# Performance work log

Measured on AMD Instinct MI355X. Metric: run time of the kernel, lower is better.

Reference implementation:

```python
import jax, jax.numpy as jnp
import numpy as np

H = 32          # query heads
KV = 8          # key/value heads
HD = 128        # head_dim
EPS = 1e-6
SCALE = HD ** -0.5


def _rms_norm(x, w):
    # per-head RMSNorm over last dim in fp32
    xf = x.astype(jnp.float32)
    var = jnp.mean(xf * xf, axis=-1, keepdims=True)
    return (w * (xf * jax.lax.rsqrt(var + EPS))).astype(x.dtype)


def _rotate_half(x):
    x1, x2 = jnp.split(x, 2, axis=-1)
    return jnp.concatenate([-x2, x1], axis=-1)


def setup_inputs() -> dict:
    key = jax.random.key(0)
    ks = jax.random.split(key, 8)
    B, S, D = 1, 2048, 4096
    hidden_states = jax.random.normal(ks[0], (B, S, D), dtype=jnp.float32)
    # rotary tables (half head dim), realistic frequencies
    pos = jnp.arange(S, dtype=jnp.float32)
    inv_freq = 1.0 / (1e6 ** (jnp.arange(0, HD, 2, dtype=jnp.float32) / HD))
    ang = pos[:, None] * inv_freq[None, :]          # [S, HD/2]
    cos = jnp.broadcast_to(jnp.cos(ang)[None], (B, S, HD // 2))
    sin = jnp.broadcast_to(jnp.sin(ang)[None], (B, S, HD // 2))
    # additive causal mask [B,1,S,S]
    causal = jnp.tril(jnp.ones((S, S), dtype=bool))
    attention_mask = jnp.where(causal, 0.0, -1e9).astype(jnp.float32)[None, None]
    attention_mask = jnp.broadcast_to(attention_mask, (B, 1, S, S))
    std = 0.02
    Wq = jax.random.normal(ks[1], (H * HD, D), dtype=jnp.float32) * std
    Wk = jax.random.normal(ks[2], (KV * HD, D), dtype=jnp.float32) * std
    Wv = jax.random.normal(ks[3], (KV * HD, D), dtype=jnp.float32) * std
    Wo = jax.random.normal(ks[4], (D, H * HD), dtype=jnp.float32) * std
    q_norm_w = jnp.ones((HD,), dtype=jnp.float32)
    k_norm_w = jnp.ones((HD,), dtype=jnp.float32)
    return {"hidden_states": hidden_states, "cos": cos, "sin": sin,
            "attention_mask": attention_mask, "Wq": Wq, "Wk": Wk, "Wv": Wv,
            "Wo": Wo, "q_norm_w": q_norm_w, "k_norm_w": k_norm_w}


def reference(hidden_states, cos, sin, attention_mask, Wq, Wk, Wv, Wo, q_norm_w, k_norm_w):
    B, S, D = hidden_states.shape
    # QKV projections (no bias), reshape to heads, per-head RMSNorm on q/k
    q = (hidden_states @ Wq.T).reshape(B, S, H, HD)
    k = (hidden_states @ Wk.T).reshape(B, S, KV, HD)
    v = (hidden_states @ Wv.T).reshape(B, S, KV, HD)
    q = _rms_norm(q, q_norm_w).transpose(0, 2, 1, 3)   # [B,H,S,HD]
    k = _rms_norm(k, k_norm_w).transpose(0, 2, 1, 3)   # [B,KV,S,HD]
    v = v.transpose(0, 2, 1, 3)                        # [B,KV,S,HD]
    # RoPE: cos/sin [B,S,HD/2] -> [B,1,S,HD]
    cos2 = jnp.concatenate([cos, cos], axis=-1)[:, None]
    sin2 = jnp.concatenate([sin, sin], axis=-1)[:, None]
    q = q * cos2 + _rotate_half(q) * sin2
    k = k * cos2 + _rotate_half(k) * sin2
    # GQA repeat kv
    n_rep = H // KV
    k = jnp.repeat(k, n_rep, axis=1)                   # [B,H,S,HD]
    v = jnp.repeat(v, n_rep, axis=1)
    # eager attention, fp32 softmax
    scores = jnp.einsum('bhqd,bhkd->bhqk', q, k) * SCALE + attention_mask
    probs = jax.nn.softmax(scores.astype(jnp.float32), axis=-1).astype(q.dtype)
    attn = jnp.einsum('bhqk,bhkd->bhqd', probs, v)
    attn = attn.transpose(0, 2, 1, 3).reshape(B, S, H * HD)
    return attn @ Wo.T
```

## Files before the change

### kernel.cpp

```cpp
#include <hip/hip_runtime.h>
#include <hip/hip_bf16.h>


#define S_LEN 2048
#define D_MODEL 4096
#define NH 32
#define NKV 8
#define HD 128
#define EPS 1e-6f
#define SCALE 0.08838834764831845f
#define NEG_BIG (-1e30f)

typedef __bf16 bf16_t;
typedef __bf16 bf16x8 __attribute__((ext_vector_type(8)));
typedef __bf16 bf16x4 __attribute__((ext_vector_type(4)));
typedef float f32x4 __attribute__((ext_vector_type(4)));

__device__ __forceinline__ bool input_is_bf16(const void* qw) {
    return ((*(const unsigned*)qw) & 0xFFFFu) == 0x3F80u;
}

__device__ __forceinline__ void gload_lds16(const void* g, void* l) {
    __builtin_amdgcn_global_load_lds(
        (const __attribute__((address_space(1))) void*)g,
        (__attribute__((address_space(3))) void*)l, 16, 0, 0);
}

template<bool BF16>
__device__ __forceinline__ float ld1(const void* p, size_t i) {
    if constexpr (BF16) return (float)((const bf16_t*)p)[i];
    else return ((const float*)p)[i];
}
template<bool BF16>
__device__ __forceinline__ void st1(void* p, size_t i, float v) {
    if constexpr (BF16) ((bf16_t*)p)[i] = (bf16_t)v;
    else ((float*)p)[i] = v;
}

__device__ __forceinline__ bf16x8 cvt8(const float* src) {
    float4 a = *(const float4*)src, b = *(const float4*)(src + 4);
    bf16x8 r;
    r[0] = (bf16_t)a.x; r[1] = (bf16_t)a.y; r[2] = (bf16_t)a.z; r[3] = (bf16_t)a.w;
    r[4] = (bf16_t)b.x; r[5] = (bf16_t)b.y; r[6] = (bf16_t)b.z; r[7] = (bf16_t)b.w;
    return r;
}

__global__ __launch_bounds__(256) void conv_kernel(const void* src, const void* qw,
                                                   bf16_t* __restrict__ dst) {
    size_t i = ((size_t)blockIdx.x * 256 + threadIdx.x) * 8;
    if (input_is_bf16(qw)) {
        *(bf16x8*)&dst[i] = *(const bf16x8*)((const bf16_t*)src + i);
    } else {
        *(bf16x8*)&dst[i] = cvt8((const float*)src + i);
    }
}

template<bool BF16>
__device__ __forceinline__ void stage_b(const void* W, size_t nrow0, int k0,
                                        bf16_t* lds_b, int tid, int lane, int w) {
    if constexpr (BF16) {
        const bf16_t* Wb = (const bf16_t*)W + nrow0 * D_MODEL;
        #pragma unroll
        for (int i = 0; i < 2; ++i) {
            int r16 = w * 2 + i;
            gload_lds16(Wb + (size_t)(r16 * 16 + (lane >> 2)) * D_MODEL + k0 + (lane & 3) * 8,
                        &lds_b[r16 * 512]);
        }
    } else {
        const float* Wf = (const float*)W + nrow0 * D_MODEL;
        #pragma unroll
        for (int j = 0; j < 2; ++j) {
            int e = j * 2048 + tid * 8;
            int row = e >> 5, kk = e & 31;
            *(bf16x8*)&lds_b[e] = cvt8(Wf + (size_t)row * D_MODEL + k0 + kk);
        }
    }
}

template<bool BF16>
__device__ void qkv_body(
    const bf16_t* __restrict__ hsb, const void* cosp, const void* sinp,
    const void* Wq, const void* Wk, const void* Wv,
    const void* qw, const void* kw,
    bf16_t* __restrict__ qn, bf16_t* __restrict__ kn, bf16_t* __restrict__ vt,
    bf16_t* lds_a, bf16_t* lds_b)
{
    const int tid = threadIdx.x;
    const int lane = tid & 63;
    const int w = tid >> 6;
    const int c = lane & 15;
    const int g = lane >> 4;
    const int m0 = blockIdx.x * 128;
    const int slot = blockIdx.y;

    const void* Wbase; int type, h;
    if (slot < 32)      { type = 0; h = slot;      Wbase = Wq; }
    else if (slot < 40) { type = 1; h = slot - 32; Wbase = Wk; }
    else                { type = 2; h = slot - 40; Wbase = Wv; }
    const size_t nrow0 = (size_t)h * HD;

    f32x4 acc[2][8] = {};

    for (int k0 = 0; k0 < D_MODEL; k0 += 32) {
        __syncthreads();
        #pragma unroll
        for (int i = 0; i < 2; ++i) {
            int r16 = w * 2 + i;
            gload_lds16(hsb + (size_t)(m0 + r16 * 16 + (lane >> 2)) * D_MODEL + k0 + (lane & 3) * 8,
                        &lds_a[r16 * 512]);
        }
        stage_b<BF16>(Wbase, nrow0, k0, lds_b, tid, lane, w);
        __syncthreads();

        bf16x8 af0 = *(const bf16x8*)&lds_a[(w * 32 + c) * 32 + g * 8];
        bf16x8 af1 = *(const bf16x8*)&lds_a[(w * 32 + 16 + c) * 32 + g * 8];
        #pragma unroll
        for (int ni = 0; ni < 8; ++ni) {
            bf16x8 bfr = *(const bf16x8*)&lds_b[(ni * 16 + c) * 32 + g * 8];
            acc[0][ni] = __builtin_amdgcn_mfma_f32_16x16x32_bf16(af0, bfr, acc[0][ni], 0, 0, 0);
            acc[1][ni] = __builtin_amdgcn_mfma_f32_16x16x32_bf16(af1, bfr, acc[1][ni], 0, 0, 0);
        }
    }

    if (type == 2) {
        #pragma unroll
        for (int mi = 0; mi < 2; ++mi) {
            int s = m0 + w * 32 + mi * 16 + g * 4;
            #pragma unroll
            for (int ni = 0; ni < 8; ++ni) {
                bf16x4 pk;
                #pragma unroll
                for (int r = 0; r < 4; ++r) pk[r] = (bf16_t)acc[mi][ni][r];
                *(bf16x4*)&vt[((size_t)h * HD + ni * 16 + c) * S_LEN + s] = pk;
            }
        }
        return;
    }

    const void* nw = (type == 0) ? qw : kw;
    bf16_t* outb = (type == 0) ? (qn + (size_t)h * S_LEN * HD)
                               : (kn + (size_t)h * S_LEN * HD);
    #pragma unroll
    for (int mi = 0; mi < 2; ++mi) {
        float ss[4];
        #pragma unroll
        for (int r = 0; r < 4; ++r) {
            float p = 0.f;
            #pragma unroll
            for (int ni = 0; ni < 8; ++ni) p += acc[mi][ni][r] * acc[mi][ni][r];
            p += __shfl_xor(p, 1); p += __shfl_xor(p, 2);
            p += __shfl_xor(p, 4); p += __shfl_xor(p, 8);
            ss[r] = rsqrtf(p * (1.f / HD) + EPS);
        }
        float v[8][4];
        #pragma unroll
        for (int ni = 0; ni < 8; ++ni) {
            float wg = ld1<BF16>(nw, ni * 16 + c);
            #pragma unroll
            for (int r = 0; r < 4; ++r) v[ni][r] = acc[mi][ni][r] * ss[r] * wg;
        }
        #pragma unroll
        for (int r = 0; r < 4; ++r) {
            int s = m0 + w * 32 + mi * 16 + g * 4 + r;
            #pragma unroll
            for (int t = 0; t < 4; ++t) {
                int nn = t * 16 + c;
                float co = ld1<BF16>(cosp, (size_t)s * 64 + nn);
                float si = ld1<BF16>(sinp, (size_t)s * 64 + nn);
                float x1 = v[t][r], x2 = v[t + 4][r];
                v[t][r]     = x1 * co - x2 * si;
                v[t + 4][r] = x2 * co + x1 * si;
            }
        }
        #pragma unroll
        for (int t = 0; t < 8; ++t)
            #pragma unroll
            for (int r = 0; r < 4; ++r) {
                int s = m0 + w * 32 + mi * 16 + g * 4 + r;
                outb[(size_t)s * HD + t * 16 + c] = (bf16_t)v[t][r];
            }
    }
}

__global__ __launch_bounds__(256) void qkv_kernel(
    const bf16_t* __restrict__ hsb, const void* cosp, const void* sinp,
    const void* Wq, const void* Wk, const void* Wv,
    const void* qw, const void* kw,
    bf16_t* __restrict__ qn, bf16_t* __restrict__ kn, bf16_t* __restrict__ vt)
{
    __shared__ bf16_t lds_a[128 * 32];
    __shared__ bf16_t lds_b[128 * 32];
    if (input_is_bf16(qw))
        qkv_body<true>(hsb, cosp, sinp, Wq, Wk, Wv, qw, kw, qn, kn, vt, lds_a, lds_b);
    else
        qkv_body<false>(hsb, cosp, sinp, Wq, Wk, Wv, qw, kw, qn, kn, vt, lds_a, lds_b);
}

__global__ __launch_bounds__(256) void attn_kernel(
    const bf16_t* __restrict__ qn, const bf16_t* __restrict__ kn,
    const bf16_t* __restrict__ vt, bf16_t* __restrict__ attnb)
{
    __shared__ bf16_t lds_k[32 * 128];
    __shared__ bf16_t lds_v[128 * 32];

    const int lane = threadIdx.x & 63;
    const int w = threadIdx.x >> 6;
    const int c = lane & 15;
    const int g = lane >> 4;
    const int h = blockIdx.y;
    const int hk = h >> 2;
    const int xa = blockIdx.x;
    const int lr = lane >> 2;
    const int lk = (lane & 3) * 8;

    const int qrow0 = xa * 64 + w * 16;
    const int qrow1 = (31 - xa) * 64 + w * 16;
    const int kmaxA = xa * 64 + 64;
    const int kmaxB = (31 - xa) * 64 + 64;

    const bf16_t* kb_base = kn + (size_t)hk * S_LEN * HD;
    const bf16_t* vt_base = vt + (size_t)hk * HD * S_LEN;

    bf16x8 qf[2][4];
    #pragma unroll
    for (int ks = 0; ks < 4; ++ks) {
        qf[0][ks] = *(const bf16x8*)(qn + ((size_t)h * S_LEN + qrow0 + c) * HD + ks * 32 + g * 8);
        qf[1][ks] = *(const bf16x8*)(qn + ((size_t)h * S_LEN + qrow1 + c) * HD + ks * 32 + g * 8);
    }

    f32x4 o[2][8] = {};
    float m_cur[2] = {NEG_BIG, NEG_BIG};
    float l_cur[2] = {0.f, 0.f};

    for (int kb = 0; kb < kmaxB; kb += 32) {
        const bool liveA = (kb < kmaxA);
        __syncthreads();
        #pragma unroll
        for (int i = 0; i < 2; ++i) {
            int t16 = w * 2 + i;
            gload_lds16(kb_base + (size_t)(kb + t16 * 4 + g) * HD + c * 8,
                        &lds_k[t16 * 512]);
            gload_lds16(vt_base + (size_t)(t16 * 16 + lr) * S_LEN + kb + lk,
                        &lds_v[t16 * 512]);
        }
        __syncthreads();

        float p[2][2][4];
        #pragma unroll
        for (int u = 0; u < 2; ++u) {
            f32x4 sacc0 = {}, sacc1 = {};
            #pragma unroll
            for (int ks = 0; ks < 4; ++ks) {
                bf16x8 kf = *(const bf16x8*)&lds_k[(u * 16 + c) * 128 + ks * 32 + g * 8];
                if (liveA)
                    sacc0 = __builtin_amdgcn_mfma_f32_16x16x32_bf16(kf, qf[0][ks], sacc0, 0, 0, 0);
                sacc1 = __builtin_amdgcn_mfma_f32_16x16x32_bf16(kf, qf[1][ks], sacc1, 0, 0, 0);
            }
            #pragma unroll
            for (int r = 0; r < 4; ++r) {
                int key_abs = kb + u * 16 + g * 4 + r;
                p[0][u][r] = (key_abs <= qrow0 + c) ? sacc0[r] * SCALE : NEG_BIG;
                p[1][u][r] = (key_abs <= qrow1 + c) ? sacc1[r] * SCALE : NEG_BIG;
            }
        }

        bf16x8 pb[2];
        #pragma unroll
        for (int qt = 0; qt < 2; ++qt) {
            if (qt == 0 && !liveA) continue;
            float mx = NEG_BIG;
            #pragma unroll
            for (int u = 0; u < 2; ++u)
                #pragma unroll
                for (int r = 0; r < 4; ++r) mx = fmaxf(mx, p[qt][u][r]);
            mx = fmaxf(mx, __shfl_xor(mx, 16));
            mx = fmaxf(mx, __shfl_xor(mx, 32));
            float m_new = fmaxf(m_cur[qt], mx);
            float alpha = __expf(m_cur[qt] - m_new);
            float lsum = 0.f;
            #pragma unroll
            for (int u = 0; u < 2; ++u)
                #pragma unroll
                for (int r = 0; r < 4; ++r) {
                    float e = __expf(p[qt][u][r] - m_new);
                    p[qt][u][r] = e;
                    lsum += e;
                }
            lsum += __shfl_xor(lsum, 16);
            lsum += __shfl_xor(lsum, 32);
            l_cur[qt] = l_cur[qt] * alpha + lsum;
            m_cur[qt] = m_new;
            #pragma unroll
            for (int dt = 0; dt < 8; ++dt) o[qt][dt] *= alpha;
            #pragma unroll
            for (int j = 0; j < 8; ++j) {
                int src = (((g * 2 + (j >> 2)) & 3) << 4) | c;
                float v0 = __shfl(p[qt][0][j & 3], src);
                float v1 = __shfl(p[qt][1][j & 3], src);
                pb[qt][j] = (bf16_t)((g >= 2) ? v1 : v0);
            }
        }
        #pragma unroll
        for (int dt = 0; dt < 8; ++dt) {
            bf16x8 vf = *(const bf16x8*)&lds_v[(dt * 16 + c) * 32 + g * 8];
            if (liveA)
                o[0][dt] = __builtin_amdgcn_mfma_f32_16x16x32_bf16(vf, pb[0], o[0][dt], 0, 0, 0);
            o[1][dt] = __builtin_amdgcn_mfma_f32_16x16x32_bf16(vf, pb[1], o[1][dt], 0, 0, 0);
        }
    }

    #pragma unroll
    for (int qt = 0; qt < 2; ++qt) {
        float inv_l = 1.f / l_cur[qt];
        int q = (qt == 0 ? qrow0 : qrow1) + c;
        #pragma unroll
        for (int dt = 0; dt < 8; ++dt) {
            bf16x4 pk;
            #pragma unroll
            for (int r = 0; r < 4; ++r) pk[r] = (bf16_t)(o[qt][dt][r] * inv_l);
            *(bf16x4*)&attnb[(size_t)q * D_MODEL + h * HD + dt * 16 + g * 4] = pk;
        }
    }
}

template<bool BF16>
__device__ void out_body(const bf16_t* __restrict__ attnb, const void* Wo,
                         void* outp, bf16_t* lds_a, bf16_t* lds_b)
{
    const int tid = threadIdx.x;
    const int lane = tid & 63;
    const int w = tid >> 6;
    const int c = lane & 15;
    const int g = lane >> 4;
    const int wm = w >> 1, wn = w & 1;
    const int m0 = blockIdx.x * 128, n0 = blockIdx.y * 128;

    f32x4 acc[4][4] = {};
    for (int k0 = 0; k0 < D_MODEL; k0 += 32) {
        __syncthreads();
        #pragma unroll
        for (int i = 0; i < 2; ++i) {
            int r16 = w * 2 + i;
            gload_lds16(attnb + (size_t)(m0 + r16 * 16 + (lane >> 2)) * D_MODEL + k0 + (lane & 3) * 8,
                        &lds_a[r16 * 512]);
        }
        stage_b<BF16>(Wo, (size_t)n0, k0, lds_b, tid, lane, w);
        __syncthreads();

        bf16x8 af[4], bfr[4];
        #pragma unroll
        for (int i = 0; i < 4; ++i) {
            af[i]  = *(const bf16x8*)&lds_a[(wm * 64 + i * 16 + c) * 32 + g * 8];
            bfr[i] = *(const bf16x8*)&lds_b[(wn * 64 + i * 16 + c) * 32 + g * 8];
        }
        #pragma unroll
        for (int mi = 0; mi < 4; ++mi)
            #pragma unroll
            for (int ni = 0; ni < 4; ++ni)
                acc[mi][ni] = __builtin_amdgcn_mfma_f32_16x16x32_bf16(af[mi], bfr[ni], acc[mi][ni], 0, 0, 0);
    }
    #pragma unroll
    for (int mi = 0; mi < 4; ++mi)
        #pragma unroll
        for (int ni = 0; ni < 4; ++ni)
            #pragma unroll
            for (int r = 0; r < 4; ++r)
                st1<BF16>(outp, (size_t)(m0 + wm * 64 + mi * 16 + g * 4 + r) * D_MODEL
                                 + n0 + wn * 64 + ni * 16 + c, acc[mi][ni][r]);
}

__global__ __launch_bounds__(256) void out_kernel(
    const bf16_t* __restrict__ attnb, const void* Wo, const void* qw, void* outp)
{
    __shared__ bf16_t lds_a[128 * 32];
    __shared__ bf16_t lds_b[128 * 32];
    if (input_is_bf16(qw)) out_body<true>(attnb, Wo, outp, lds_a, lds_b);
    else                   out_body<false>(attnb, Wo, outp, lds_a, lds_b);
}

extern "C" void kernel_launch(void* const* d_in, const int* in_sizes, int n_in,
                              void* d_out, int out_size, void* d_ws, size_t ws_size,
                              hipStream_t stream) {
    const void* hs   = d_in[0];
    const void* cosp = d_in[1];
    const void* sinp = d_in[2];
    const void* Wq = d_in[4];
    const void* Wk = d_in[5];
    const void* Wv = d_in[6];
    const void* Wo = d_in[7];
    const void* qw = d_in[8];
    const void* kw = d_in[9];

    const size_t NEED = 16777216ull + 16777216ull + 4194304ull + 4194304ull;
    if (ws_size < NEED) return;

    char* ws = (char*)d_ws;
    bf16_t* buf0 = (bf16_t*)(ws);
    bf16_t* qn   = (bf16_t*)(ws + 16777216);
    bf16_t* kn   = (bf16_t*)(ws + 2 * 16777216);
    bf16_t* vt   = (bf16_t*)(ws + 2 * 16777216 + 4194304);

    conv_kernel<<<dim3(4096), 256, 0, stream>>>(hs, qw, buf0);
    qkv_kernel<<<dim3(16, 48), 256, 0, stream>>>(buf0, cosp, sinp, Wq, Wk, Wv, qw, kw,
                                                 qn, kn, vt);
    attn_kernel<<<dim3(16, 32), 256, 0, stream>>>(qn, kn, vt, buf0);
    out_kernel<<<dim3(16, 32), 256, 0, stream>>>(buf0, Wo, qw, d_out);
}
```

Baseline: 762.4 us.

## Pre-convert weights to bf16 and double-buffer LDS in GEMM kernels

Adds a kernel that converts Wq, Wk, Wv and Wo to bf16 in workspace once per call. The QKV and output GEMMs can then stage weights with direct global-to-LDS loads instead of converting fp32 inline in every block. Both GEMM loops also get double-buffered LDS so the next K-tile loads while the current one computes, dropping one barrier per iteration. The cost is an extra full read and write pass over all weights per call, a larger workspace requirement, and double the LDS footprint, which may lower occupancy.

```diff
diff --git a/kernel.cpp b/kernel.cpp
--- a/kernel.cpp
+++ b/kernel.cpp
@@ -55,10 +55,38 @@
     }
 }
 
-template<bool BF16>
-__device__ __forceinline__ void stage_b(const void* W, size_t nrow0, int k0,
+__global__ __launch_bounds__(256) void convw_kernel(
+    const void* Wq, const void* Wk, const void* Wv, const void* Wo,
+    const void* qw, bf16_t* __restrict__ dq, bf16_t* __restrict__ dk,
+    bf16_t* __restrict__ dv, bf16_t* __restrict__ dwo) {
+    int b = blockIdx.x;
+    const void* src; bf16_t* dst; size_t base;
+    if (b < 8192)       { src = Wq; dst = dq;  base = (size_t)b * 2048; }
+    else if (b < 10240) { src = Wk; dst = dk;  base = (size_t)(b - 8192) * 2048; }
+    else if (b < 12288) { src = Wv; dst = dv;  base = (size_t)(b - 10240) * 2048; }
+    else                { src = Wo; dst = dwo; base = (size_t)(b - 12288) * 2048; }
+    size_t i = base + (size_t)threadIdx.x * 8;
+    if (input_is_bf16(qw)) {
+        *(bf16x8*)&dst[i] = *(const bf16x8*)((const bf16_t*)src + i);
+    } else {
+        *(bf16x8*)&dst[i] = cvt8((const float*)src + i);
+    }
+}
+
+__device__ __forceinline__ void stage_a(const bf16_t* __restrict__ src, int m0,
+                                        int k0, bf16_t* lds_a, int lane, int w) {
+    #pragma unroll
+    for (int i = 0; i < 2; ++i) {
+        int r16 = w * 2 + i;
+        gload_lds16(src + (size_t)(m0 + r16 * 16 + (lane >> 2)) * D_MODEL + k0 + (lane & 3) * 8,
+                    &lds_a[r16 * 512]);
+    }
+}
+
+template<bool WB>
+__device__ __forceinline__ void stage_w(const void* W, size_t nrow0, int k0,
                                         bf16_t* lds_b, int tid, int lane, int w) {
-    if constexpr (BF16) {
+    if constexpr (WB) {
         const bf16_t* Wb = (const bf16_t*)W + nrow0 * D_MODEL;
         #pragma unroll
         for (int i = 0; i < 2; ++i) {
@@ -77,7 +105,7 @@
     }
 }
 
-template<bool BF16>
+template<bool BF16, bool WB>
 __device__ void qkv_body(
     const bf16_t* __restrict__ hsb, const void* cosp, const void* sinp,
     const void* Wq, const void* Wk, const void* Wv,
@@ -101,25 +129,29 @@
 
     f32x4 acc[2][8] = {};
 
+    stage_a(hsb, m0, 0, lds_a, lane, w);
+    stage_w<WB>(Wbase, nrow0, 0, lds_b, tid, lane, w);
+    __syncthreads();
+
+    int cur = 0;
     for (int k0 = 0; k0 < D_MODEL; k0 += 32) {
-        __syncthreads();
-        #pragma unroll
-        for (int i = 0; i < 2; ++i) {
-            int r16 = w * 2 + i;
-            gload_lds16(hsb + (size_t)(m0 + r16 * 16 + (lane >> 2)) * D_MODEL + k0 + (lane & 3) * 8,
-                        &lds_a[r16 * 512]);
-        }
-        stage_b<BF16>(Wbase, nrow0, k0, lds_b, tid, lane, w);
-        __syncthreads();
-
-        bf16x8 af0 = *(const bf16x8*)&lds_a[(w * 32 + c) * 32 + g * 8];
-        bf16x8 af1 = *(const bf16x8*)&lds_a[(w * 32 + 16 + c) * 32 + g * 8];
+        int nxt = cur ^ 1;
+        if (k0 + 32 < D_MODEL) {
+            stage_a(hsb, m0, k0 + 32, lds_a + nxt * 4096, lane, w);
+            stage_w<WB>(Wbase, nrow0, k0 + 32, lds_b + nxt * 4096, tid, lane, w);
+        }
+        const bf16_t* la = lds_a + cur * 4096;
+        const bf16_t* lb = lds_b + cur * 4096;
+        bf16x8 af0 = *(const bf16x8*)&la[(w * 32 + c) * 32 + g * 8];
+        bf16x8 af1 = *(const bf16x8*)&la[(w * 32 + 16 + c) * 32 + g * 8];
         #pragma unroll
         for (int ni = 0; ni < 8; ++ni) {
-            bf16x8 bfr = *(const bf16x8*)&lds_b[(ni * 16 + c) * 32 + g * 8];
+            bf16x8 bfr = *(const bf16x8*)&lb[(ni * 16 + c) * 32 + g * 8];
             acc[0][ni] = __builtin_amdgcn_mfma_f32_16x16x32_bf16(af0, bfr, acc[0][ni], 0, 0, 0);
             acc[1][ni] = __builtin_amdgcn_mfma_f32_16x16x32_bf16(af1, bfr, acc[1][ni], 0, 0, 0);
         }
+        __syncthreads();
+        cur = nxt;
     }
 
     if (type == 2) {
@@ -186,14 +218,19 @@
     const bf16_t* __restrict__ hsb, const void* cosp, const void* sinp,
     const void* Wq, const void* Wk, const void* Wv,
     const void* qw, const void* kw,
-    bf16_t* __restrict__ qn, bf16_t* __restrict__ kn, bf16_t* __restrict__ vt)
+    bf16_t* __restrict__ qn, bf16_t* __restrict__ kn, bf16_t* __restrict__ vt,
+    int wconv)
 {
-    __shared__ bf16_t lds_a[128 * 32];
-    __shared__ bf16_t lds_b[128 * 32];
-    if (input_is_bf16(qw))
-        qkv_body<true>(hsb, cosp, sinp, Wq, Wk, Wv, qw, kw, qn, kn, vt, lds_a, lds_b);
-    else
-        qkv_body<false>(hsb, cosp, sinp, Wq, Wk, Wv, qw, kw, qn, kn, vt, lds_a, lds_b);
+    __shared__ bf16_t lds_a[2][128 * 32];
+    __shared__ bf16_t lds_b[2][128 * 32];
+    bool ib = input_is_bf16(qw);
+    if (wconv) {
+        if (ib) qkv_body<true,  true>(hsb, cosp, sinp, Wq, Wk, Wv, qw, kw, qn, kn, vt, &lds_a[0][0], &lds_b[0][0]);
+        else    qkv_body<false, true>(hsb, cosp, sinp, Wq, Wk, Wv, qw, kw, qn, kn, vt, &lds_a[0][0], &lds_b[0][0]);
+    } else {
+        if (ib) qkv_body<true,  true>(hsb, cosp, sinp, Wq, Wk, Wv, qw, kw, qn, kn, vt, &lds_a[0][0], &lds_b[0][0]);
+        else    qkv_body<false, false>(hsb, cosp, sinp, Wq, Wk, Wv, qw, kw, qn, kn, vt, &lds_a[0][0], &lds_b[0][0]);
+    }
 }
 
 __global__ __launch_bounds__(256) void attn_kernel(
@@ -323,7 +360,7 @@
     }
 }
 
-template<bool BF16>
+template<bool BF16, bool WB>
 __device__ void out_body(const bf16_t* __restrict__ attnb, const void* Wo,
                          void* outp, bf16_t* lds_a, bf16_t* lds_b)
 {
@@ -336,28 +373,33 @@
     const int m0 = blockIdx.x * 128, n0 = blockIdx.y * 128;
 
     f32x4 acc[4][4] = {};
+
+    stage_a(attnb, m0, 0, lds_a, lane, w);
+    stage_w<WB>(Wo, (size_t)n0, 0, lds_b, tid, lane, w);
+    __syncthreads();
+
+    int cur = 0;
     for (int k0 = 0; k0 < D_MODEL; k0 += 32) {
-        __syncthreads();
-        #pragma unroll
-        for (int i = 0; i < 2; ++i) {
-            int r16 = w * 2 + i;
-            gload_lds16(attnb + (size_t)(m0 + r16 * 16 + (lane >> 2)) * D_MODEL + k0 + (lane & 3) * 8,
-                        &lds_a[r16 * 512]);
-        }
-        stage_b<BF16>(Wo, (size_t)n0, k0, lds_b, tid, lane, w);
-        __syncthreads();
-
+        int nxt = cur ^ 1;
+        if (k0 + 32 < D_MODEL) {
+            stage_a(attnb, m0, k0 + 32, lds_a + nxt * 4096, lane, w);
+            stage_w<WB>(Wo, (size_t)n0, k0 + 32, lds_b + nxt * 4096, tid, lane, w);
+        }
+        const bf16_t* la = lds_a + cur * 4096;
+        const bf16_t* lb = lds_b + cur * 4096;
         bf16x8 af[4], bfr[4];
         #pragma unroll
         for (int i = 0; i < 4; ++i) {
-            af[i]  = *(const bf16x8*)&lds_a[(wm * 64 + i * 16 + c) * 32 + g * 8];
-            bfr[i] = *(const bf16x8*)&lds_b[(wn * 64 + i * 16 + c) * 32 + g * 8];
+            af[i]  = *(const bf16x8*)&la[(wm * 64 + i * 16 + c) * 32 + g * 8];
+            bfr[i] = *(const bf16x8*)&lb[(wn * 64 + i * 16 + c) * 32 + g * 8];
         }
         #pragma unroll
         for (int mi = 0; mi < 4; ++mi)
             #pragma unroll
             for (int ni = 0; ni < 4; ++ni)
                 acc[mi][ni] = __builtin_amdgcn_mfma_f32_16x16x32_bf16(af[mi], bfr[ni], acc[mi][ni], 0, 0, 0);
+        __syncthreads();
+        cur = nxt;
     }
     #pragma unroll
     for (int mi = 0; mi < 4; ++mi)
@@ -370,12 +412,19 @@
 }
 
 __global__ __launch_bounds__(256) void out_kernel(
-    const bf16_t* __restrict__ attnb, const void* Wo, const void* qw, void* outp)
+    const bf16_t* __restrict__ attnb, const void* Wo, const void* qw, void* outp,
+    int wconv)
 {
-    __shared__ bf16_t lds_a[128 * 32];
-    __shared__ bf16_t lds_b[128 * 32];
-    if (input_is_bf16(qw)) out_body<true>(attnb, Wo, outp, lds_a, lds_b);
-    else                   out_body<false>(attnb, Wo, outp, lds_a, lds_b);
+    __shared__ bf16_t lds_a[2][128 * 32];
+    __shared__ bf16_t lds_b[2][128 * 32];
+    bool ib = input_is_bf16(qw);
+    if (wconv) {
+        if (ib) out_body<true,  true>(attnb, Wo, outp, &lds_a[0][0], &lds_b[0][0]);
+        else    out_body<false, true>(attnb, Wo, outp, &lds_a[0][0], &lds_b[0][0]);
+    } else {
+        if (ib) out_body<true,  true>(attnb, Wo, outp, &lds_a[0][0], &lds_b[0][0]);
+        else    out_body<false, false>(attnb, Wo, outp, &lds_a[0][0], &lds_b[0][0]);
+    }
 }
 
 extern "C" void kernel_launch(void* const* d_in, const int* in_sizes, int n_in,
@@ -391,8 +440,10 @@
     const void* qw = d_in[8];
     const void* kw = d_in[9];
 
-    const size_t NEED = 16777216ull + 16777216ull + 4194304ull + 4194304ull;
+    const size_t NEED   = 41943040ull;
+    const size_t NEED_W = NEED + 83886080ull;
     if (ws_size < NEED) return;
+    const int wconv = (ws_size >= NEED_W) ? 1 : 0;
 
     char* ws = (char*)d_ws;
     bf16_t* buf0 = (bf16_t*)(ws);
@@ -401,8 +452,21 @@
     bf16_t* vt   = (bf16_t*)(ws + 2 * 16777216 + 4194304);
 
     conv_kernel<<<dim3(4096), 256, 0, stream>>>(hs, qw, buf0);
-    qkv_kernel<<<dim3(16, 48), 256, 0, stream>>>(buf0, cosp, sinp, Wq, Wk, Wv, qw, kw,
-                                                 qn, kn, vt);
-    attn_kernel<<<dim3(16, 32), 256, 0, stream>>>(qn, kn, vt, buf0);
-    out_kernel<<<dim3(16, 32), 256, 0, stream>>>(buf0, Wo, qw, d_out);
-}
+
+    if (wconv) {
+        bf16_t* dq  = (bf16_t*)(ws + NEED);
+        bf16_t* dk  = (bf16_t*)(ws + NEED + 33554432ull);
+        bf16_t* dv  = (bf16_t*)(ws + NEED + 33554432ull + 8388608ull);
+        bf16_t* dwo = (bf16_t*)(ws + NEED + 33554432ull + 2*8388608ull);
+        convw_kernel<<<dim3(20480), 256, 0, stream>>>(Wq, Wk, Wv, Wo, qw, dq, dk, dv, dwo);
+        qkv_kernel<<<dim3(16, 48), 256, 0, stream>>>(buf0, cosp, sinp, dq, dk, dv, qw, kw,
+                                                     qn, kn, vt, 1);
+        attn_kernel<<<dim3(16, 32), 256, 0, stream>>>(qn, kn, vt, buf0);
+        out_kernel<<<dim3(16, 32), 256, 0, stream>>>(buf0, dwo, qw, d_out, 1);
+    } else {
+        qkv_kernel<<<dim3(16, 48), 256, 0, stream>>>(buf0, cosp, sinp, Wq, Wk, Wv, qw, kw,
+                                                     qn, kn, vt, 0);
+        attn_kernel<<<dim3(16, 32), 256, 0, stream>>>(qn, kn, vt, buf0);
+        out_kernel<<<dim3(16, 32), 256, 0, stream>>>(buf0, Wo, qw, d_out, 0);
+    }
+}
```

After: 727.3 us. 4.6% less time.
